# Kernel tuning notes

Hardware: AMD Instinct MI355X
Metric: run time of the kernel (lower is better)

The kernel has to match this reference:

```python
import jax, jax.numpy as jnp
import numpy as np

L = 8            # gat_blocks(4) * layers(2)
LAYERS = 2
RC, DC, SC, EC = 32, 32, 256, 512
IN_DIM, OUT_DIM = 2, 12
N_NODES, EMB, D_ATT = 512, 16, 16
B, T_IN = 8, 13  # T_IN == receptive_field -> no left padding


def setup_inputs() -> dict:
    key = jax.random.key(0)
    ks = jax.random.split(key, 12)
    g = lambda k, shp: jax.random.normal(k, shp, jnp.float32) * 0.05
    return {
        "input": jax.random.normal(ks[0], (B, IN_DIM, N_NODES, T_IN), jnp.float32),
        "gat_supports": jax.random.normal(ks[1], (EMB, N_NODES), jnp.float32),
        "start_w": g(ks[2], (RC, IN_DIM)), "start_b": jnp.zeros((RC,), jnp.float32),
        "filt_w": g(ks[3], (L, DC, RC, 1, 2)), "filt_b": jnp.zeros((L, DC), jnp.float32),
        "gate_w": g(ks[4], (L, DC, RC, 1, 2)), "gate_b": jnp.zeros((L, DC), jnp.float32),
        "skip_w": g(ks[5], (L, SC, DC)), "skip_b": jnp.zeros((L, SC), jnp.float32),
        "q_w": g(ks[6], (L, D_ATT, DC + EMB)), "q_b": jnp.zeros((L, D_ATT), jnp.float32),
        "k_w": g(ks[7], (L, D_ATT, DC + EMB)), "k_b": jnp.zeros((L, D_ATT), jnp.float32),
        "gmlp_w": g(ks[8], (L, RC, 2 * DC)), "gmlp_b": jnp.zeros((L, RC), jnp.float32),
        "bn_g": jnp.ones((L, RC), jnp.float32), "bn_b": jnp.zeros((L, RC), jnp.float32),
        "end1_w": g(ks[9], (EC, SC)), "end1_b": jnp.zeros((EC,), jnp.float32),
        "end2_w": g(ks[10], (OUT_DIM, EC)), "end2_b": jnp.zeros((OUT_DIM,), jnp.float32),
    }


def _pw(x, w, b):
    # 1x1 conv (pointwise linear over channels): x [B,C,N,T], w [O,C]
    return jnp.einsum('oc,bcnt->bont', w, x) + b[None, :, None, None]


def _tconv(x, w, b, d):
    # dilated temporal conv, kernel (1,2), VALID (shrinks T by d)
    y = jax.lax.conv_general_dilated(
        x, w, window_strides=(1, 1), padding='VALID', rhs_dilation=(1, d),
        dimension_numbers=('NCHW', 'OIHW', 'NCHW'))
    return y + b[None, :, None, None]


def _bn(x, g, b, eps=1e-5):
    # BatchNorm2d (training-mode batch stats, biased variance, as in torch)
    m = jnp.mean(x, axis=(0, 2, 3), keepdims=True)
    v = jnp.var(x, axis=(0, 2, 3), keepdims=True)
    return g[None, :, None, None] * (x - m) * jax.lax.rsqrt(v + eps) + b[None, :, None, None]


def _forward(input, gat_supports, start_w, start_b, filt_w, filt_b, gate_w, gate_b,
             skip_w, skip_b, q_w, q_b, k_w, k_b, gmlp_w, gmlp_b, bn_g, bn_b,
             end1_w, end1_b, end2_w, end2_b):
    x = _pw(input, start_w, start_b)          # [B,RC,N,T]
    skip = None
    scale = 1.0 / (D_ATT ** 0.5)
    for i in range(L):
        d = 2 ** (i % LAYERS)                 # dilation schedule 1,2 per block
        residual = x
        f = jnp.tanh(_tconv(residual, filt_w[i], filt_b[i], d))
        gt = jax.nn.sigmoid(_tconv(residual, gate_w[i], gate_b[i], d))
        x = f * gt                            # [B,DC,N,T-d]
        s = _pw(x, skip_w[i], skip_b[i])      # [B,SC,N,T-d]
        skip = s if skip is None else s + skip[:, :, :, -s.shape[3]:]
        # --- adaptive graph attention ---
        Bn, C, N, T = x.shape
        emb = jnp.broadcast_to(gat_supports[None, :, :, None], (Bn, EMB, N, T))
        xe = jnp.concatenate([x, emb], axis=1)            # [B,C+EMB,N,T]
        q = _pw(xe, q_w[i], q_b[i]).transpose(0, 3, 2, 1)  # [B,T,N,d]
        kk = _pw(xe, k_w[i], k_b[i]).transpose(0, 3, 2, 1)
        att = jax.nn.softmax(jnp.einsum('btnd,btmd->btnm', q, kk) * scale, axis=-1)
        xa = jnp.einsum('bcvt,btvw->bcwt', x, att)         # x @ att on node axis
        x = _pw(jnp.concatenate([x, xa], axis=1), gmlp_w[i], gmlp_b[i])
        # ---------------------------------
        x = x + residual[:, :, :, -x.shape[3]:]
        x = _bn(x, bn_g[i], bn_b[i])
    out = jax.nn.relu(skip)
    out = jax.nn.relu(_pw(out, end1_w, end1_b))
    out = _pw(out, end2_w, end2_b)            # [B,OUT_DIM,N,1]
    return out


def reference(input, gat_supports, start_w, start_b, filt_w, filt_b, gate_w, gate_b,
              skip_w, skip_b, q_w, q_b, k_w, k_b, gmlp_w, gmlp_b, bn_g, bn_b,
              end1_w, end1_b, end2_w, end2_b):
    return _forward(input, gat_supports, start_w, start_b, filt_w, filt_b, gate_w,
                    gate_b, skip_w, skip_b, q_w, q_b, k_w, k_b, gmlp_w, gmlp_b,
                    bn_g, bn_b, end1_w, end1_b, end2_w, end2_b)
```

## Files before the change

### kernel.cpp

```cpp
#include <hip/hip_runtime.h>
#include <math.h>


typedef short v4s __attribute__((ext_vector_type(4)));
typedef float v4f __attribute__((ext_vector_type(4)));
typedef unsigned short ushort_t;

#define MFMA16(a,b,c) __builtin_amdgcn_mfma_f32_16x16x16bf16_1k(a, b, c, 0, 0, 0)

__device__ inline ushort_t f2bf(float f){
    unsigned int u = __builtin_bit_cast(unsigned int, f);
    u += 0x7FFFu + ((u >> 16) & 1u);
    return (ushort_t)(u >> 16);
}
__device__ inline float bf2f(ushort_t h){
    return __builtin_bit_cast(float, ((unsigned int)h) << 16);
}

__global__ void k_prep(
    const float* __restrict__ inp, const float* __restrict__ start_w, const float* __restrict__ start_b,
    const float* __restrict__ gat,
    const float* __restrict__ qw, const float* __restrict__ qb,
    const float* __restrict__ kw, const float* __restrict__ kb,
    const float* __restrict__ filt_w, const float* __restrict__ gate_w,
    const float* __restrict__ skip_w,
    const float* __restrict__ w1, const float* __restrict__ w2,
    float* __restrict__ zero_base,
    float* __restrict__ qe, float* __restrict__ ke, float* __restrict__ x0,
    ushort_t* __restrict__ cwh, ushort_t* __restrict__ cwl, ushort_t* __restrict__ qkw,
    ushort_t* __restrict__ swh, ushort_t* __restrict__ swl,
    ushort_t* __restrict__ w1ph, ushort_t* __restrict__ w1pl,
    ushort_t* __restrict__ w2ph, ushort_t* __restrict__ w2pl)
{
    const int E0 = 1049024;
    const int E1 = E0 + 131072;
    const int E2 = E1 + 1703936;
    const int E3 = E2 + 32768;
    const int E4 = E3 + 8192;
    const int E5 = E4 + 65536;
    const int E6 = E5 + 131072;
    const int E7 = E6 + 8192;
    int idx = blockIdx.x*256 + threadIdx.x;
    if (idx < E0){
        zero_base[idx] = 0.0f;
    } else if (idx < E1){
        int id = idx - E0;
        const int total = 8*512*16;
        bool isK = id >= total;
        if (isK) id -= total;
        int dq = id & 15; int n = (id >> 4) & 511; int l = id >> 13;
        const float* w = isK ? kw : qw;
        const float* bi = isK ? kb : qb;
        float acc = bi[l*16 + dq];
        const float* wrow = w + (l*16 + dq)*48 + 32;
        #pragma unroll
        for (int e = 0; e < 16; e++) acc += wrow[e] * gat[e*512 + n];
        (isK ? ke : qe)[(l*512 + n)*16 + dq] = isK ? acc : acc*0.25f;
    } else if (idx < E2){
        int id = idx - E1;
        int n = id & 511; int c = (id >> 9) & 31; int r = id >> 14;
        int t = r % 13; int b = r / 13;
        float v0 = inp[((b*2 + 0)*512 + n)*13 + t];
        float v1 = inp[((b*2 + 1)*512 + n)*13 + t];
        x0[id] = start_b[c] + start_w[c*2 + 0]*v0 + start_w[c*2 + 1]*v1;
    } else if (idx < E3){
        int id = idx - E2;
        int k = id & 63, o = (id >> 6) & 63, l = id >> 12;
        int c = k & 31, tap = k >> 5;
        float w = (o < 32) ? filt_w[((l*32 + o)*32 + c)*2 + tap]
                           : gate_w[((l*32 + (o-32))*32 + c)*2 + tap];
        ushort_t hi = f2bf(w);
        cwh[id] = hi; cwl[id] = f2bf(w - bf2f(hi));
    } else if (idx < E4){
        int id = idx - E3;
        int c = id & 31, j = (id >> 5) & 31, l = id >> 10;
        float w = (j < 16) ? qw[(l*16 + j)*48 + c]*0.25f : kw[(l*16 + (j-16))*48 + c];
        qkw[id] = f2bf(w);
    } else if (idx < E5){
        int id = idx - E4;
        float w = skip_w[id];
        ushort_t hi = f2bf(w);
        swh[id] = hi; swl[id] = f2bf(w - bf2f(hi));
    } else if (idx < E6){
        int id = idx - E5;
        int j = id & 15, m16 = (id >> 4) & 15, kk = (id >> 8) & 15, ot = id >> 12;
        float w = w1[((size_t)(ot*16 + m16))*256 + kk*16 + j];
        ushort_t hi = f2bf(w);
        w1ph[id] = hi; w1pl[id] = f2bf(w - bf2f(hi));
    } else if (idx < E7){
        int id = idx - E6;
        int j = id & 15, m16 = (id >> 4) & 15, kt = id >> 8;
        float w = (m16 < 12) ? w2[m16*512 + kt*16 + j] : 0.0f;
        ushort_t hi = f2bf(w);
        w2ph[id] = hi; w2pl[id] = f2bf(w - bf2f(hi));
    }
}

__global__ __launch_bounds__(256) void k_gated_mfma(
    const float* __restrict__ xin, int Tin, int d, int Tout,
    const float* __restrict__ bnsumP, const float* __restrict__ bnG,
    const float* __restrict__ bnB, int ident, float cnt,
    const ushort_t* __restrict__ cwh, const ushort_t* __restrict__ cwl,
    const float* __restrict__ fb, const float* __restrict__ gb,
    const ushort_t* __restrict__ qkw,
    const float* __restrict__ qe, const float* __restrict__ ke,
    const ushort_t* __restrict__ swh, const ushort_t* __restrict__ swl,
    const float* __restrict__ sb,
    float* __restrict__ skip,
    ushort_t* __restrict__ xbfT, ushort_t* __restrict__ qbf, ushort_t* __restrict__ kbf,
    int do_qk)
{
    __shared__ unsigned int XBP[64*129];
    __shared__ float ABsh[64];
    int tid = threadIdx.x;
    int nch = blockIdx.x, t = blockIdx.y, b = blockIdx.z;
    size_t bt = (size_t)(b*Tout + t);
    int n0 = nch*128;
    int lane = tid & 63, wid = tid >> 6;
    int m16 = lane & 15, g4 = (lane >> 4)*4;

    if (tid < 32){
        float A, Bc;
        if (ident){ A = 1.0f; Bc = 0.0f; }
        else {
            float S = bnsumP[2*tid], S2 = bnsumP[2*tid + 1];
            float m = S/cnt, var = S2/cnt - m*m;
            A = bnG[tid]*rsqrtf(var + 1e-5f);
            Bc = bnB[tid] - m*A;
        }
        ABsh[tid] = A; ABsh[32 + tid] = Bc;
    }
    __syncthreads();

    #pragma unroll
    for (int kk = 0; kk < 16; kk++){
        int k = wid*16 + kk;
        int c = k & 31, tap = k >> 5;
        const float* src = xin + ((size_t)(b*Tin + t + tap*d)*32 + c)*512 + n0 + lane;
        float An = ABsh[c], Bn = ABsh[32 + c];
        #pragma unroll
        for (int h = 0; h < 2; h++){
            float xn = An*src[h*64] + Bn;
            ushort_t hi = f2bf(xn);
            ushort_t lo = f2bf(xn - bf2f(hi));
            XBP[k*129 + h*64 + lane] = (unsigned int)hi | ((unsigned int)lo << 16);
        }
    }
    v4s ah[4][4], al[4][4];
    #pragma unroll
    for (int ot = 0; ot < 4; ot++)
    #pragma unroll
    for (int kt = 0; kt < 4; kt++){
        ah[ot][kt] = *(const v4s*)(cwh + (ot*16 + m16)*64 + kt*16 + g4);
        al[ot][kt] = *(const v4s*)(cwl + (ot*16 + m16)*64 + kt*16 + g4);
    }
    v4f acc[4][2];
    #pragma unroll
    for (int ot = 0; ot < 4; ot++){
        float4 bv = *(const float4*)((ot < 2 ? fb + ot*16 : gb + (ot-2)*16) + g4);
        acc[ot][0] = (v4f){bv.x, bv.y, bv.z, bv.w};
        acc[ot][1] = (v4f){bv.x, bv.y, bv.z, bv.w};
    }
    __syncthreads();
    v4s bh[2][4], bl[2][4];
    #pragma unroll
    for (int nt = 0; nt < 2; nt++){
        int nl = (wid*2 + nt)*16 + m16;
        #pragma unroll
        for (int kt = 0; kt < 4; kt++){
            unsigned int u0 = XBP[(kt*16 + g4 + 0)*129 + nl];
            unsigned int u1 = XBP[(kt*16 + g4 + 1)*129 + nl];
            unsigned int u2 = XBP[(kt*16 + g4 + 2)*129 + nl];
            unsigned int u3 = XBP[(kt*16 + g4 + 3)*129 + nl];
            v4s hh, ll;
            hh[0] = (short)(u0 & 0xffffu); ll[0] = (short)(u0 >> 16);
            hh[1] = (short)(u1 & 0xffffu); ll[1] = (short)(u1 >> 16);
            hh[2] = (short)(u2 & 0xffffu); ll[2] = (short)(u2 >> 16);
            hh[3] = (short)(u3 & 0xffffu); ll[3] = (short)(u3 >> 16);
            bh[nt][kt] = hh; bl[nt][kt] = ll;
        }
    }
    #pragma unroll
    for (int kt = 0; kt < 4; kt++)
    #pragma unroll
    for (int ot = 0; ot < 4; ot++)
    #pragma unroll
    for (int nt = 0; nt < 2; nt++){
        acc[ot][nt] = MFMA16(ah[ot][kt], bh[nt][kt], acc[ot][nt]);
        acc[ot][nt] = MFMA16(ah[ot][kt], bl[nt][kt], acc[ot][nt]);
        acc[ot][nt] = MFMA16(al[ot][kt], bh[nt][kt], acc[ot][nt]);
    }
    v4s xh[2][2], xl[2][2];
    #pragma unroll
    for (int ct = 0; ct < 2; ct++)
    #pragma unroll
    for (int nt = 0; nt < 2; nt++){
        v4s hh, ll;
        #pragma unroll
        for (int i = 0; i < 4; i++){
            float f = acc[ct][nt][i], g = acc[ct+2][nt][i];
            float e2 = __expf(2.0f*f);
            float th = 1.0f - 2.0f/(e2 + 1.0f);
            float sg = 1.0f/(1.0f + __expf(-g));
            float v = th*sg;
            ushort_t hi = f2bf(v);
            hh[i] = (short)hi; ll[i] = (short)f2bf(v - bf2f(hi));
        }
        xh[ct][nt] = hh; xl[ct][nt] = ll;
    }
    if (do_qk){
        #pragma unroll
        for (int ct = 0; ct < 2; ct++)
        #pragma unroll
        for (int nt = 0; nt < 2; nt++){
            int nl = n0 + (wid*2 + nt)*16 + m16;
            #pragma unroll
            for (int i = 0; i < 4; i++)
                xbfT[(bt*32 + ct*16 + g4 + i)*512 + nl] = (ushort_t)xh[ct][nt][i];
        }
        v4s qa[2][2];
        #pragma unroll
        for (int ot = 0; ot < 2; ot++)
        #pragma unroll
        for (int kt = 0; kt < 2; kt++)
            qa[ot][kt] = *(const v4s*)(qkw + (ot*16 + m16)*32 + kt*16 + g4);
        #pragma unroll
        for (int ot = 0; ot < 2; ot++)
        #pragma unroll
        for (int nt = 0; nt < 2; nt++){
            int nl = n0 + (wid*2 + nt)*16 + m16;
            float4 ev = *(const float4*)((ot == 0 ? qe : ke) + nl*16 + g4);
            v4f a2 = (v4f){ev.x, ev.y, ev.z, ev.w};
            #pragma unroll
            for (int kt = 0; kt < 2; kt++)
                a2 = MFMA16(qa[ot][kt], xh[kt][nt], a2);
            v4s r;
            #pragma unroll
            for (int i = 0; i < 4; i++) r[i] = (short)f2bf(a2[i]);
            *(v4s*)((ot == 0 ? qbf : kbf) + (bt*512 + nl)*16 + g4) = r;
        }
    }
    if (t == Tout - 1){
        #pragma unroll 4
        for (int ot = 0; ot < 16; ot++){
            v4s sh_[2], sl_[2];
            #pragma unroll
            for (int kt = 0; kt < 2; kt++){
                sh_[kt] = *(const v4s*)(swh + (ot*16 + m16)*32 + kt*16 + g4);
                sl_[kt] = *(const v4s*)(swl + (ot*16 + m16)*32 + kt*16 + g4);
            }
            float4 sbv = *(const float4*)(sb + ot*16 + g4);
            #pragma unroll
            for (int nt = 0; nt < 2; nt++){
                int nl = n0 + (wid*2 + nt)*16 + m16;
                float* sp = skip + ((size_t)(b*512) + nl)*256 + ot*16 + g4;
                float4 old = *(const float4*)sp;
                v4f a3 = (v4f){old.x + sbv.x, old.y + sbv.y, old.z + sbv.z, old.w + sbv.w};
                #pragma unroll
                for (int kt = 0; kt < 2; kt++){
                    a3 = MFMA16(sh_[kt], xh[kt][nt], a3);
                    a3 = MFMA16(sh_[kt], xl[kt][nt], a3);
                    a3 = MFMA16(sl_[kt], xh[kt][nt], a3);
                }
                *(float4*)sp = make_float4(a3[0], a3[1], a3[2], a3[3]);
            }
        }
    }
}

__global__ __launch_bounds__(256) void k_z(
    const ushort_t* __restrict__ qbf, const ushort_t* __restrict__ kbf,
    int Tout, float* __restrict__ rz)
{
    __shared__ ushort_t KS[512*20];
    int tid = threadIdx.x;
    int vchunk = blockIdx.x, t = blockIdx.y, b = blockIdx.z;
    size_t bt = (size_t)(b*Tout + t);
    const ushort_t* kg = kbf + bt*8192;
    const ushort_t* qg = qbf + bt*8192;
    {
        const uint2* s0 = (const uint2*)(kg + tid*16);
        uint2* d0 = (uint2*)(KS + tid*20);
        d0[0]=s0[0]; d0[1]=s0[1]; d0[2]=s0[2]; d0[3]=s0[3];
        const uint2* s1 = (const uint2*)(kg + (tid+256)*16);
        uint2* d1 = (uint2*)(KS + (tid+256)*20);
        d1[0]=s1[0]; d1[1]=s1[1]; d1[2]=s1[2]; d1[3]=s1[3];
    }
    int l = tid & 63, wid = tid >> 6;
    int m16 = l & 15, g4 = (l >> 4)*4;
    __syncthreads();
    int vt = vchunk*4 + wid;
    v4s bq = *(const v4s*)(qg + (vt*16 + m16)*16 + g4);
    float zp = 0.f;
    for (int wt = 0; wt < 32; wt++){
        v4s ak = *(const v4s*)(KS + (wt*16 + m16)*20 + g4);
        v4f s = MFMA16(ak, bq, ((v4f){0.f,0.f,0.f,0.f}));
        zp += __expf(fminf(s[0],60.f)) + __expf(fminf(s[1],60.f))
            + __expf(fminf(s[2],60.f)) + __expf(fminf(s[3],60.f));
    }
    zp += __shfl_xor(zp, 16);
    zp += __shfl_xor(zp, 32);
    if (l < 16) rz[bt*512 + vt*16 + l] = 1.0f/zp;
}

__global__ __launch_bounds__(256) void k_pv(
    const ushort_t* __restrict__ qbf, const ushort_t* __restrict__ kbf,
    const ushort_t* __restrict__ xbfT, const float* __restrict__ rz,
    const float* __restrict__ xin, int Tin, int d, int Tout,
    const float* __restrict__ bnsumP, const float* __restrict__ bnG,
    const float* __restrict__ bnB, int ident, float cnt,
    const float* __restrict__ gw, const float* __restrict__ gb,
    float* __restrict__ y, float* __restrict__ bnsumOut)
{
    __shared__ ushort_t QS[512*20];
    __shared__ ushort_t XT[32*520];
    __shared__ float rzs[512];
    __shared__ float bnsh[256];
    __shared__ float ABsh[64];
    int tid = threadIdx.x;
    int wc = blockIdx.x, t = blockIdx.y, b = blockIdx.z;
    size_t bt = (size_t)(b*Tout + t);
    const ushort_t* qg = qbf + bt*8192;
    const ushort_t* kg = kbf + bt*8192;
    {
        const uint2* s0 = (const uint2*)(qg + tid*16);
        uint2* d0 = (uint2*)(QS + tid*20);
        d0[0]=s0[0]; d0[1]=s0[1]; d0[2]=s0[2]; d0[3]=s0[3];
        const uint2* s1 = (const uint2*)(qg + (tid+256)*16);
        uint2* d1 = (uint2*)(QS + (tid+256)*20);
        d1[0]=s1[0]; d1[1]=s1[1]; d1[2]=s1[2]; d1[3]=s1[3];
        int c = tid >> 3, seg = tid & 7;
        const uint4* xs = (const uint4*)(xbfT + bt*16384 + c*512 + seg*64);
        uint4* xd = (uint4*)(XT + c*520 + seg*64);
        #pragma unroll
        for (int j = 0; j < 8; j++) xd[j] = xs[j];
        rzs[tid] = rz[bt*512 + tid];
        rzs[tid + 256] = rz[bt*512 + tid + 256];
    }
    if (tid < 32){
        float A, Bc;
        if (ident){ A = 1.0f; Bc = 0.0f; }
        else {
            float S = bnsumP[2*tid], S2 = bnsumP[2*tid + 1];
            float m = S/cnt, var = S2/cnt - m*m;
            A = bnG[tid]*rsqrtf(var + 1e-5f);
            Bc = bnB[tid] - m*A;
        }
        ABsh[tid] = A; ABsh[32 + tid] = Bc;
    }
    int l = tid & 63, wid = tid >> 6;
    int m16 = l & 15, g4 = (l >> 4)*4;
    v4s AG[2][2][2];
    #pragma unroll
    for (int pt = 0; pt < 2; pt++)
    #pragma unroll
    for (int ot = 0; ot < 2; ot++)
    #pragma unroll
    for (int ct = 0; ct < 2; ct++){
        float4 gv = *(const float4*)(gw + (ot*16 + m16)*64 + pt*32 + ct*16 + g4);
        v4s r; r[0] = (short)f2bf(gv.x); r[1] = (short)f2bf(gv.y);
        r[2] = (short)f2bf(gv.z); r[3] = (short)f2bf(gv.w);
        AG[pt][ot][ct] = r;
    }
    v4f gbv[2];
    #pragma unroll
    for (int ot = 0; ot < 2; ot++) gbv[ot] = *(const v4f*)(gb + ot*16 + g4);
    int wt = wc*4 + wid;
    v4s bk = *(const v4s*)(kg + (wt*16 + m16)*16 + g4);
    __syncthreads();
    v4f An[2], Bn[2];
    #pragma unroll
    for (int ot = 0; ot < 2; ot++){
        #pragma unroll
        for (int i = 0; i < 4; i++){
            An[ot][i] = ABsh[ot*16 + g4 + i];
            Bn[ot][i] = ABsh[32 + ot*16 + g4 + i];
        }
    }
    v4f c2[2];
    c2[0] = (v4f){0.f,0.f,0.f,0.f}; c2[1] = (v4f){0.f,0.f,0.f,0.f};
    for (int vt = 0; vt < 32; vt++){
        v4s aq = *(const v4s*)(QS + (vt*16 + m16)*20 + g4);
        v4f s0 = MFMA16(aq, bk, ((v4f){0.f,0.f,0.f,0.f}));
        v4f rzv = *(const v4f*)(rzs + vt*16 + g4);
        v4s p0;
        #pragma unroll
        for (int i = 0; i < 4; i++)
            p0[i] = (short)f2bf(__expf(fminf(s0[i],60.f)) * rzv[i]);
        #pragma unroll
        for (int ct = 0; ct < 2; ct++){
            v4s ax = *(const v4s*)(XT + (ct*16 + m16)*520 + vt*16 + g4);
            c2[ct] = MFMA16(ax, p0, c2[ct]);
        }
    }
    float bs1[2][4], bs2[2][4];
    #pragma unroll
    for (int ot = 0; ot < 2; ot++)
    #pragma unroll
    for (int i = 0; i < 4; i++){ bs1[ot][i] = 0.f; bs2[ot][i] = 0.f; }
    {
        v4s bxa[2], bx[2];
        #pragma unroll
        for (int ct = 0; ct < 2; ct++){
            v4s r;
            #pragma unroll
            for (int i = 0; i < 4; i++) r[i] = (short)f2bf(c2[ct][i]);
            bxa[ct] = r;
            v4s q;
            #pragma unroll
            for (int i = 0; i < 4; i++) q[i] = (short)XT[(ct*16 + g4 + i)*520 + wt*16 + m16];
            bx[ct] = q;
        }
        v4f c3[2];
        #pragma unroll
        for (int ot = 0; ot < 2; ot++){
            c3[ot] = gbv[ot];
            #pragma unroll
            for (int ct = 0; ct < 2; ct++){
                c3[ot] = MFMA16(AG[1][ot][ct], bxa[ct], c3[ot]);
                c3[ot] = MFMA16(AG[0][ot][ct], bx[ct],  c3[ot]);
            }
        }
        int wg = wt*16 + m16;
        const float* resbase = xin + ((size_t)(b*Tin + t + d)*32)*512 + wg;
        float* ybase = y + (bt*32)*512 + wg;
        #pragma unroll
        for (int ot = 0; ot < 2; ot++){
            #pragma unroll
            for (int i = 0; i < 4; i++){
                int outc = ot*16 + g4 + i;
                float yv = c3[ot][i] + An[ot][i]*resbase[(size_t)outc*512] + Bn[ot][i];
                ybase[(size_t)outc*512] = yv;
                bs1[ot][i] += yv; bs2[ot][i] += yv*yv;
            }
        }
    }
    #pragma unroll
    for (int off = 1; off <= 8; off <<= 1){
        #pragma unroll
        for (int ot = 0; ot < 2; ot++)
        #pragma unroll
        for (int i = 0; i < 4; i++){
            bs1[ot][i] += __shfl_xor(bs1[ot][i], off);
            bs2[ot][i] += __shfl_xor(bs2[ot][i], off);
        }
    }
    if (m16 == 0){
        #pragma unroll
        for (int ot = 0; ot < 2; ot++)
        #pragma unroll
        for (int i = 0; i < 4; i++){
            int c = ot*16 + g4 + i;
            bnsh[(wid*32 + c)*2 + 0] = bs1[ot][i];
            bnsh[(wid*32 + c)*2 + 1] = bs2[ot][i];
        }
    }
    __syncthreads();
    if (tid < 64){
        int c = tid & 31, p = tid >> 5;
        float s = 0.f;
        #pragma unroll
        for (int w = 0; w < 4; w++) s += bnsh[(w*32 + c)*2 + p];
        atomicAdd(&bnsumOut[c*2 + p], s);
    }
}

__global__ __launch_bounds__(256) void k_end_all(
    const float* __restrict__ skip,
    const ushort_t* __restrict__ w1ph, const ushort_t* __restrict__ w1pl,
    const float* __restrict__ b1,
    const ushort_t* __restrict__ w2ph, const ushort_t* __restrict__ w2pl,
    const float* __restrict__ b2, float* __restrict__ out)
{
    __shared__ ushort_t SH[16*264], SL[16*264];
    __shared__ ushort_t HH[512*18], HL[512*18];
    __shared__ float PS[4][16][17];
    int tid = threadIdx.x;
    int nc = blockIdx.x, b = blockIdx.y;
    int n0 = nc*16;
    {
        int n = tid >> 4, s = tid & 15;
        const float4* src = (const float4*)(skip + ((size_t)(b*512 + n0 + n))*256 + s*16);
        #pragma unroll
        for (int j = 0; j < 4; j++){
            float4 v4_ = src[j];
            float vv[4] = {v4_.x, v4_.y, v4_.z, v4_.w};
            #pragma unroll
            for (int e = 0; e < 4; e++){
                float v = fmaxf(vv[e], 0.f);
                ushort_t h = f2bf(v);
                SH[n*264 + s*16 + j*4 + e] = h;
                SL[n*264 + s*16 + j*4 + e] = f2bf(v - bf2f(h));
            }
        }
    }
    __syncthreads();
    int l = tid & 63, wid = tid >> 6;
    int m16 = l & 15, g4 = (l >> 4)*4;
    v4f acc[8];
    #pragma unroll
    for (int nt = 0; nt < 8; nt++){
        float bo = b1[(wid*8 + nt)*16 + m16];
        acc[nt] = (v4f){bo, bo, bo, bo};
    }
    for (int kk = 0; kk < 16; kk++){
        v4s ahi = *(const v4s*)(SH + m16*264 + kk*16 + g4);
        v4s alo = *(const v4s*)(SL + m16*264 + kk*16 + g4);
        #pragma unroll
        for (int nt = 0; nt < 8; nt++){
            int ob = ((wid*8 + nt)*16 + kk)*256;
            v4s bhi = *(const v4s*)(w1ph + ob + m16*16 + g4);
            v4s blo = *(const v4s*)(w1pl + ob + m16*16 + g4);
            acc[nt] = MFMA16(ahi, bhi, acc[nt]);
            acc[nt] = MFMA16(ahi, blo, acc[nt]);
            acc[nt] = MFMA16(alo, bhi, acc[nt]);
        }
    }
    #pragma unroll
    for (int nt = 0; nt < 8; nt++){
        int o = (wid*8 + nt)*16 + m16;
        #pragma unroll
        for (int i = 0; i < 4; i++){
            float v = fmaxf(acc[nt][i], 0.f);
            ushort_t h = f2bf(v);
            HH[o*18 + g4 + i] = h;
            HL[o*18 + g4 + i] = f2bf(v - bf2f(h));
        }
    }
    __syncthreads();
    v4f a4 = (v4f){0.f, 0.f, 0.f, 0.f};
    for (int q = 0; q < 8; q++){
        int kt = wid*8 + q;
        v4s wh = *(const v4s*)(w2ph + kt*256 + m16*16 + g4);
        v4s wl = *(const v4s*)(w2pl + kt*256 + m16*16 + g4);
        v4s hh, hl;
        #pragma unroll
        for (int i = 0; i < 4; i++){
            int k = kt*16 + g4 + i;
            hh[i] = (short)HH[k*18 + m16];
            hl[i] = (short)HL[k*18 + m16];
        }
        a4 = MFMA16(wh, hh, a4);
        a4 = MFMA16(wh, hl, a4);
        a4 = MFMA16(wl, hh, a4);
    }
    #pragma unroll
    for (int i = 0; i < 4; i++) PS[wid][g4 + i][m16] = a4[i];
    __syncthreads();
    if (wid == 0){
        #pragma unroll
        for (int i = 0; i < 4; i++){
            int od = g4 + i;
            if (od < 12){
                float v = b2[od] + PS[0][od][m16] + PS[1][od][m16]
                        + PS[2][od][m16] + PS[3][od][m16];
                out[((size_t)(b*12 + od))*512 + n0 + m16] = v;
            }
        }
    }
}

extern "C" void kernel_launch(void* const* d_in, const int* in_sizes, int n_in,
                              void* d_out, int out_size, void* d_ws, size_t ws_size,
                              hipStream_t stream)
{
    (void)in_sizes; (void)n_in; (void)out_size; (void)ws_size;
    const float* input  = (const float*)d_in[0];
    const float* gat    = (const float*)d_in[1];
    const float* start_w= (const float*)d_in[2];
    const float* start_b= (const float*)d_in[3];
    const float* filt_w = (const float*)d_in[4];
    const float* filt_b = (const float*)d_in[5];
    const float* gate_w = (const float*)d_in[6];
    const float* gate_b = (const float*)d_in[7];
    const float* skip_w = (const float*)d_in[8];
    const float* skip_b = (const float*)d_in[9];
    const float* q_w    = (const float*)d_in[10];
    const float* q_b    = (const float*)d_in[11];
    const float* k_w    = (const float*)d_in[12];
    const float* k_b    = (const float*)d_in[13];
    const float* gmlp_w = (const float*)d_in[14];
    const float* gmlp_b = (const float*)d_in[15];
    const float* bn_g   = (const float*)d_in[16];
    const float* bn_b   = (const float*)d_in[17];
    const float* end1_w = (const float*)d_in[18];
    const float* end1_b = (const float*)d_in[19];
    const float* end2_w = (const float*)d_in[20];
    const float* end2_b = (const float*)d_in[21];
    float* out = (float*)d_out;

    float* W = (float*)d_ws;
    size_t off = 0;
    float* skip = W + off; off += (size_t)8*512*256;
    float* bnsum= W + off; off += (size_t)7*64;
    float* bufA = W + off; off += (size_t)8*13*32*512;
    float* bufB = W + off; off += (size_t)8*13*32*512;
    float* qe   = W + off; off += (size_t)8*512*16;
    float* ke   = W + off; off += (size_t)8*512*16;
    float* rz   = W + off; off += (size_t)8*12*512;
    ushort_t* xbfT = (ushort_t*)(W + off); off += (size_t)8*12*32*512/2;
    ushort_t* qbf  = (ushort_t*)(W + off); off += (size_t)8*12*512*16/2;
    ushort_t* kbf  = (ushort_t*)(W + off); off += (size_t)8*12*512*16/2;
    ushort_t* cwh  = (ushort_t*)(W + off); off += (size_t)32768/2;
    ushort_t* cwl  = (ushort_t*)(W + off); off += (size_t)32768/2;
    ushort_t* qkw  = (ushort_t*)(W + off); off += (size_t)8192/2;
    ushort_t* swbh = (ushort_t*)(W + off); off += (size_t)65536/2;
    ushort_t* swbl = (ushort_t*)(W + off); off += (size_t)65536/2;
    ushort_t* w1ph = (ushort_t*)(W + off); off += (size_t)512*256/2;
    ushort_t* w1pl = (ushort_t*)(W + off); off += (size_t)512*256/2;
    ushort_t* w2ph = (ushort_t*)(W + off); off += (size_t)16*512/2;
    ushort_t* w2pl = (ushort_t*)(W + off); off += (size_t)16*512/2;

    k_prep<<<12226, 256, 0, stream>>>(input, start_w, start_b, gat,
        q_w, q_b, k_w, k_b, filt_w, gate_w, skip_w, end1_w, end2_w,
        skip, qe, ke, bufA,
        cwh, cwl, qkw, swbh, swbl, w1ph, w1pl, w2ph, w2pl);

    const int Tin[8] = {13,12,10,9,7,6,4,3};
    const int Dd[8]  = {1,2,1,2,1,2,1,2};
    float* xin = bufA; float* yb = bufB;
    for (int i = 0; i < 8; i++){
        int Ti = Tin[i], d = Dd[i], To = Ti - d;
        const float* bnsumP = (i == 0) ? bnsum : bnsum + (i-1)*64;
        const float* gP = (i == 0) ? bn_g : bn_g + (i-1)*32;
        const float* bP = (i == 0) ? bn_b : bn_b + (i-1)*32;
        int ident = (i == 0) ? 1 : 0;
        float cnt = 8.0f * (float)Ti * 512.0f;
        k_gated_mfma<<<dim3(4, To, 8), 256, 0, stream>>>(xin, Ti, d, To,
            bnsumP, gP, bP, ident, cnt,
            cwh + i*4096, cwl + i*4096, filt_b + i*32, gate_b + i*32,
            qkw + i*1024, qe + i*8192, ke + i*8192,
            swbh + i*8192, swbl + i*8192, skip_b + i*256,
            skip, xbfT, qbf, kbf, (i < 7) ? 1 : 0);
        if (i < 7){
            k_z<<<dim3(8, To, 8), 256, 0, stream>>>(qbf, kbf, To, rz);
            k_pv<<<dim3(8, To, 8), 256, 0, stream>>>(qbf, kbf, xbfT, rz,
                xin, Ti, d, To, bnsumP, gP, bP, ident, cnt,
                gmlp_w + i*2048, gmlp_b + i*32, yb, bnsum + i*64);
            float* tmp = xin; xin = yb; yb = tmp;
        }
    }
    k_end_all<<<dim3(32, 8), 256, 0, stream>>>(skip, w1ph, w1pl, end1_b, w2ph, w2pl, end2_b, out);
}
```

Baseline: 443.8 us.

## Fuse softmax normalizer and PV kernels with in-block redundant row sums

```diff
diff --git a/kernel.cpp b/kernel.cpp
--- a/kernel.cpp
+++ b/kernel.cpp
@@ -83,14 +83,14 @@
         swh[id] = hi; swl[id] = f2bf(w - bf2f(hi));
     } else if (idx < E6){
         int id = idx - E5;
-        int j = id & 15, m16 = (id >> 4) & 15, kk = (id >> 8) & 15, ot = id >> 12;
-        float w = w1[((size_t)(ot*16 + m16))*256 + kk*16 + j];
+        int j = id & 15, mm = (id >> 4) & 15, kk = (id >> 8) & 15, ot = id >> 12;
+        float w = w1[((size_t)(ot*16 + mm))*256 + kk*16 + j];
         ushort_t hi = f2bf(w);
         w1ph[id] = hi; w1pl[id] = f2bf(w - bf2f(hi));
     } else if (idx < E7){
         int id = idx - E6;
-        int j = id & 15, m16 = (id >> 4) & 15, kt = id >> 8;
-        float w = (m16 < 12) ? w2[m16*512 + kt*16 + j] : 0.0f;
+        int j = id & 15, mm = (id >> 4) & 15, kt = id >> 8;
+        float w = (mm < 12) ? w2[mm*512 + kt*16 + j] : 0.0f;
         ushort_t hi = f2bf(w);
         w2ph[id] = hi; w2pl[id] = f2bf(w - bf2f(hi));
     }
@@ -268,60 +268,29 @@
     }
 }
 
-__global__ __launch_bounds__(256) void k_z(
+__global__ __launch_bounds__(256) void k_zpv(
     const ushort_t* __restrict__ qbf, const ushort_t* __restrict__ kbf,
-    int Tout, float* __restrict__ rz)
-{
-    __shared__ ushort_t KS[512*20];
-    int tid = threadIdx.x;
-    int vchunk = blockIdx.x, t = blockIdx.y, b = blockIdx.z;
-    size_t bt = (size_t)(b*Tout + t);
-    const ushort_t* kg = kbf + bt*8192;
-    const ushort_t* qg = qbf + bt*8192;
-    {
-        const uint2* s0 = (const uint2*)(kg + tid*16);
-        uint2* d0 = (uint2*)(KS + tid*20);
-        d0[0]=s0[0]; d0[1]=s0[1]; d0[2]=s0[2]; d0[3]=s0[3];
-        const uint2* s1 = (const uint2*)(kg + (tid+256)*16);
-        uint2* d1 = (uint2*)(KS + (tid+256)*20);
-        d1[0]=s1[0]; d1[1]=s1[1]; d1[2]=s1[2]; d1[3]=s1[3];
-    }
-    int l = tid & 63, wid = tid >> 6;
-    int m16 = l & 15, g4 = (l >> 4)*4;
-    __syncthreads();
-    int vt = vchunk*4 + wid;
-    v4s bq = *(const v4s*)(qg + (vt*16 + m16)*16 + g4);
-    float zp = 0.f;
-    for (int wt = 0; wt < 32; wt++){
-        v4s ak = *(const v4s*)(KS + (wt*16 + m16)*20 + g4);
-        v4f s = MFMA16(ak, bq, ((v4f){0.f,0.f,0.f,0.f}));
-        zp += __expf(fminf(s[0],60.f)) + __expf(fminf(s[1],60.f))
-            + __expf(fminf(s[2],60.f)) + __expf(fminf(s[3],60.f));
-    }
-    zp += __shfl_xor(zp, 16);
-    zp += __shfl_xor(zp, 32);
-    if (l < 16) rz[bt*512 + vt*16 + l] = 1.0f/zp;
-}
-
-__global__ __launch_bounds__(256) void k_pv(
-    const ushort_t* __restrict__ qbf, const ushort_t* __restrict__ kbf,
-    const ushort_t* __restrict__ xbfT, const float* __restrict__ rz,
+    const ushort_t* __restrict__ xbfT,
     const float* __restrict__ xin, int Tin, int d, int Tout,
     const float* __restrict__ bnsumP, const float* __restrict__ bnG,
     const float* __restrict__ bnB, int ident, float cnt,
     const float* __restrict__ gw, const float* __restrict__ gb,
     float* __restrict__ y, float* __restrict__ bnsumOut)
 {
-    __shared__ ushort_t QS[512*20];
-    __shared__ ushort_t XT[32*520];
-    __shared__ float rzs[512];
-    __shared__ float bnsh[256];
-    __shared__ float ABsh[64];
+    __shared__ __align__(16) char LB[77568];
+    ushort_t* KS = (ushort_t*)LB;
+    ushort_t* QS = (ushort_t*)(LB + 20480);
+    ushort_t* XT = (ushort_t*)(LB + 40960);
+    float* rzs   = (float*)(LB + 74240);
+    float* bnsh  = (float*)(LB + 76288);
+    float* ABsh  = (float*)(LB + 77312);
     int tid = threadIdx.x;
     int wc = blockIdx.x, t = blockIdx.y, b = blockIdx.z;
     size_t bt = (size_t)(b*Tout + t);
     const ushort_t* qg = qbf + bt*8192;
     const ushort_t* kg = kbf + bt*8192;
+    int lane = tid & 63, wid = tid >> 6;
+    int m16 = lane & 15, g4 = (lane >> 4)*4;
     {
         const uint2* s0 = (const uint2*)(qg + tid*16);
         uint2* d0 = (uint2*)(QS + tid*20);
@@ -329,13 +298,17 @@
         const uint2* s1 = (const uint2*)(qg + (tid+256)*16);
         uint2* d1 = (uint2*)(QS + (tid+256)*20);
         d1[0]=s1[0]; d1[1]=s1[1]; d1[2]=s1[2]; d1[3]=s1[3];
+        const uint2* s2 = (const uint2*)(kg + tid*16);
+        uint2* d2 = (uint2*)(KS + tid*20);
+        d2[0]=s2[0]; d2[1]=s2[1]; d2[2]=s2[2]; d2[3]=s2[3];
+        const uint2* s3 = (const uint2*)(kg + (tid+256)*16);
+        uint2* d3 = (uint2*)(KS + (tid+256)*20);
+        d3[0]=s3[0]; d3[1]=s3[1]; d3[2]=s3[2]; d3[3]=s3[3];
         int c = tid >> 3, seg = tid & 7;
         const uint4* xs = (const uint4*)(xbfT + bt*16384 + c*512 + seg*64);
         uint4* xd = (uint4*)(XT + c*520 + seg*64);
         #pragma unroll
         for (int j = 0; j < 8; j++) xd[j] = xs[j];
-        rzs[tid] = rz[bt*512 + tid];
-        rzs[tid + 256] = rz[bt*512 + tid + 256];
     }
     if (tid < 32){
         float A, Bc;
@@ -348,8 +321,6 @@
         }
         ABsh[tid] = A; ABsh[32 + tid] = Bc;
     }
-    int l = tid & 63, wid = tid >> 6;
-    int m16 = l & 15, g4 = (l >> 4)*4;
     v4s AG[2][2][2];
     #pragma unroll
     for (int pt = 0; pt < 2; pt++)
@@ -365,9 +336,25 @@
     v4f gbv[2];
     #pragma unroll
     for (int ot = 0; ot < 2; ot++) gbv[ot] = *(const v4f*)(gb + ot*16 + g4);
-    int wt = wc*4 + wid;
-    v4s bk = *(const v4s*)(kg + (wt*16 + m16)*16 + g4);
-    __syncthreads();
+    __syncthreads();
+
+    #pragma unroll
+    for (int vi = 0; vi < 8; vi++){
+        int vt = wid*8 + vi;
+        v4s bq = *(const v4s*)(QS + (vt*16 + m16)*20 + g4);
+        float zp = 0.f;
+        for (int wt = 0; wt < 32; wt++){
+            v4s ak = *(const v4s*)(KS + (wt*16 + m16)*20 + g4);
+            v4f s = MFMA16(ak, bq, ((v4f){0.f,0.f,0.f,0.f}));
+            zp += __expf(fminf(s[0],60.f)) + __expf(fminf(s[1],60.f))
+                + __expf(fminf(s[2],60.f)) + __expf(fminf(s[3],60.f));
+        }
+        zp += __shfl_xor(zp, 16);
+        zp += __shfl_xor(zp, 32);
+        if (lane < 16) rzs[vt*16 + lane] = 1.0f/zp;
+    }
+    __syncthreads();
+
     v4f An[2], Bn[2];
     #pragma unroll
     for (int ot = 0; ot < 2; ot++){
@@ -377,20 +364,29 @@
             Bn[ot][i] = ABsh[32 + ot*16 + g4 + i];
         }
     }
-    v4f c2[2];
-    c2[0] = (v4f){0.f,0.f,0.f,0.f}; c2[1] = (v4f){0.f,0.f,0.f,0.f};
+    int wt0 = wc*8 + wid*2;
+    v4s bk[2];
+    bk[0] = *(const v4s*)(KS + (wt0*16 + m16)*20 + g4);
+    bk[1] = *(const v4s*)(KS + ((wt0+1)*16 + m16)*20 + g4);
+    v4f c2[2][2];
+    #pragma unroll
+    for (int i = 0; i < 2; i++){ c2[i][0] = (v4f){0.f,0.f,0.f,0.f}; c2[i][1] = (v4f){0.f,0.f,0.f,0.f}; }
     for (int vt = 0; vt < 32; vt++){
         v4s aq = *(const v4s*)(QS + (vt*16 + m16)*20 + g4);
-        v4f s0 = MFMA16(aq, bk, ((v4f){0.f,0.f,0.f,0.f}));
+        v4f s0 = MFMA16(aq, bk[0], ((v4f){0.f,0.f,0.f,0.f}));
+        v4f s1 = MFMA16(aq, bk[1], ((v4f){0.f,0.f,0.f,0.f}));
         v4f rzv = *(const v4f*)(rzs + vt*16 + g4);
-        v4s p0;
-        #pragma unroll
-        for (int i = 0; i < 4; i++)
+        v4s p0, p1;
+        #pragma unroll
+        for (int i = 0; i < 4; i++){
             p0[i] = (short)f2bf(__expf(fminf(s0[i],60.f)) * rzv[i]);
+            p1[i] = (short)f2bf(__expf(fminf(s1[i],60.f)) * rzv[i]);
+        }
         #pragma unroll
         for (int ct = 0; ct < 2; ct++){
             v4s ax = *(const v4s*)(XT + (ct*16 + m16)*520 + vt*16 + g4);
-            c2[ct] = MFMA16(ax, p0, c2[ct]);
+            c2[0][ct] = MFMA16(ax, p0, c2[0][ct]);
+            c2[1][ct] = MFMA16(ax, p1, c2[1][ct]);
         }
     }
     float bs1[2][4], bs2[2][4];
@@ -398,13 +394,15 @@
     for (int ot = 0; ot < 2; ot++)
     #pragma unroll
     for (int i = 0; i < 4; i++){ bs1[ot][i] = 0.f; bs2[ot][i] = 0.f; }
-    {
+    #pragma unroll
+    for (int wtl = 0; wtl < 2; wtl++){
+        int wt = wt0 + wtl;
         v4s bxa[2], bx[2];
         #pragma unroll
         for (int ct = 0; ct < 2; ct++){
             v4s r;
             #pragma unroll
-            for (int i = 0; i < 4; i++) r[i] = (short)f2bf(c2[ct][i]);
+            for (int i = 0; i < 4; i++) r[i] = (short)f2bf(c2[wtl][ct][i]);
             bxa[ct] = r;
             v4s q;
             #pragma unroll
@@ -457,11 +455,11 @@
     }
     __syncthreads();
     if (tid < 64){
-        int c = tid & 31, p = tid >> 5;
+        int c = tid & 31, pp = tid >> 5;
         float s = 0.f;
         #pragma unroll
-        for (int w = 0; w < 4; w++) s += bnsh[(w*32 + c)*2 + p];
-        atomicAdd(&bnsumOut[c*2 + p], s);
+        for (int w = 0; w < 4; w++) s += bnsh[(w*32 + c)*2 + pp];
+        atomicAdd(&bnsumOut[c*2 + pp], s);
     }
 }
 
@@ -597,7 +595,6 @@
     float* bufB = W + off; off += (size_t)8*13*32*512;
     float* qe   = W + off; off += (size_t)8*512*16;
     float* ke   = W + off; off += (size_t)8*512*16;
-    float* rz   = W + off; off += (size_t)8*12*512;
     ushort_t* xbfT = (ushort_t*)(W + off); off += (size_t)8*12*32*512/2;
     ushort_t* qbf  = (ushort_t*)(W + off); off += (size_t)8*12*512*16/2;
     ushort_t* kbf  = (ushort_t*)(W + off); off += (size_t)8*12*512*16/2;
@@ -633,8 +630,7 @@
             swbh + i*8192, swbl + i*8192, skip_b + i*256,
             skip, xbfT, qbf, kbf, (i < 7) ? 1 : 0);
         if (i < 7){
-            k_z<<<dim3(8, To, 8), 256, 0, stream>>>(qbf, kbf, To, rz);
-            k_pv<<<dim3(8, To, 8), 256, 0, stream>>>(qbf, kbf, xbfT, rz,
+            k_zpv<<<dim3(4, To, 8), 256, 0, stream>>>(qbf, kbf, xbfT,
                 xin, Ti, d, To, bnsumP, gP, bP, ident, cnt,
                 gmlp_w + i*2048, gmlp_b + i*32, yb, bnsum + i*64);
             float* tmp = xin; xin = yb; yb = tmp;
```

Measured after the change: 529.8 us. 19.4% more time.
